# Kernel tuning notes

Measured on AMD Instinct MI355X. Metric: run time of the kernel, lower is better.

Reference implementation:

```python
import jax, jax.numpy as jnp
import numpy as np
import math

EMBED = 1024
HEADS = 16
HEAD_DIM = EMBED // HEADS


def setup_inputs() -> dict:
    key = jax.random.key(0)
    k1, k2, k3 = jax.random.split(key, 3)
    B, C, N = 2, EMBED, 2048
    x = jax.random.normal(k1, (B, C, N), dtype=jnp.float32)
    # Conv1d(kernel_size=1, bias=False) weights, stored as [out_ch, in_ch]
    fan = 1.0 / math.sqrt(EMBED)
    w_qkv = jax.random.uniform(k2, (3 * EMBED, EMBED), dtype=jnp.float32, minval=-fan, maxval=fan)
    w_out = jax.random.uniform(k3, (EMBED, EMBED), dtype=jnp.float32, minval=-fan, maxval=fan)
    return {"x": x, "w_qkv": w_qkv, "w_out": w_out}


def reference(x, w_qkv, w_out):
    B, C, N = x.shape
    H, HD = HEADS, HEAD_DIM
    # 1x1 conv == channel matmul: [B, 3E, N]
    qkv = jnp.einsum('oc,bcn->bon', w_qkv, x)
    # permute -> [B, N, 3E]; reshape splits 3E as (H, 3*HD) per original code
    qkv = qkv.transpose(0, 2, 1).reshape(B, N, H, 3 * HD)
    qkv = qkv.transpose(0, 2, 1, 3)  # [B, H, N, 3*HD]
    q, k, v = jnp.split(qkv, 3, axis=-1)  # each [B, H, N, HD]
    scale = 1.0 / math.sqrt(HD)
    scores = jnp.einsum('bhnd,bhmd->bhnm', q, k) * scale
    weight = jax.nn.softmax(scores, axis=-1)
    vals = jnp.einsum('bhnm,bhmd->bhnd', weight, v)
    vals = vals.transpose(0, 2, 1, 3).reshape(B, N, C)  # [B, N, C]
    y = jnp.einsum('oc,bnc->bon', w_out, vals)  # [B, C, N]
    return y
```

## Files before the change

### kernel.cpp

```cpp
#include <hip/hip_runtime.h>
#include <stdint.h>

typedef unsigned short u16;
typedef __attribute__((ext_vector_type(8))) short bf16x8;
typedef __attribute__((ext_vector_type(4))) float f32x4;

#define NSEQ  2048
#define EMBED 1024
#define NHEAD 16
#define HDIM  64
#define QSCALE 0.1803368801111204f

__device__ __forceinline__ u16 f2bf(float f) {
  uint32_t u = __builtin_bit_cast(uint32_t, f);
  u += 0x7fffu + ((u >> 16) & 1u);
  return (u16)(u >> 16);
}

__device__ __forceinline__ uint32_t pk2(float a, float b) {
  return (uint32_t)f2bf(a) | ((uint32_t)f2bf(b) << 16);
}

__device__ __forceinline__ void gl_lds16(const void* g, void* l) {
  __builtin_amdgcn_global_load_lds(
      (const __attribute__((address_space(1))) void*)g,
      (__attribute__((address_space(3))) void*)l, 16, 0, 0);
}

struct alignas(8) us4 { u16 a, b, c, d; };

__global__ __launch_bounds__(256)
void convertw(const float* __restrict__ wq, const float* __restrict__ wo,
              u16* __restrict__ oq, u16* __restrict__ oo) {
  int idx = blockIdx.x * 256 + threadIdx.x;
  const float* src;
  u16* dst;
  if (idx < 786432) { src = wq; dst = oq; }
  else { idx -= 786432; src = wo; dst = oo; }
  f32x4 v = ((const f32x4*)src)[idx];
  us4 r;
  r.a = f2bf(v[0]); r.b = f2bf(v[1]); r.c = f2bf(v[2]); r.d = f2bf(v[3]);
  ((us4*)dst)[idx] = r;
}

__global__ __launch_bounds__(256)
void transpose_x(const float* __restrict__ x, u16* __restrict__ xT) {
  __shared__ float tile[32][33];
  const int b = blockIdx.z;
  const int n0 = blockIdx.x * 32, c0 = blockIdx.y * 32;
  const int tx = threadIdx.x & 31, ty = threadIdx.x >> 5;
  const float* xb = x + (size_t)b * EMBED * NSEQ;
  #pragma unroll
  for (int k = 0; k < 4; ++k)
    tile[ty + k * 8][tx] = xb[(size_t)(c0 + ty + k * 8) * NSEQ + n0 + tx];
  __syncthreads();
  u16* xTb = xT + (size_t)b * NSEQ * EMBED;
  #pragma unroll
  for (int k = 0; k < 4; ++k)
    xTb[(size_t)(n0 + ty + k * 8) * EMBED + c0 + tx] = f2bf(tile[tx][ty + k * 8]);
}

template<int EPI>
__global__ __launch_bounds__(256, 2)
void gemm_bt(const u16* __restrict__ A, const u16* __restrict__ Bm,
             u16* __restrict__ o_q, u16* __restrict__ o_k, u16* __restrict__ o_vt,
             float* __restrict__ o_f)
{
  __shared__ u16 lA[128 * 64];
  __shared__ u16 lB[128 * 64];
  const int t  = threadIdx.x;
  const int w  = t >> 6;
  const int l  = t & 63;
  const int lr = l & 15, lh = l >> 4;
  const int wm = w >> 1, wn = w & 1;
  const int bz = blockIdx.z;
  const int m0 = blockIdx.x * 128;
  const int n0 = blockIdx.y * 128;

  const u16* Ab = A  + (EPI == 0 ? (size_t)bz * NSEQ * EMBED : (size_t)0);
  const u16* Bb = Bm + (EPI == 0 ? (size_t)0 : (size_t)bz * NSEQ * EMBED);

  f32x4 acc[4][4];
  #pragma unroll
  for (int i = 0; i < 4; ++i)
    #pragma unroll
    for (int j = 0; j < 4; ++j)
      acc[i][j] = (f32x4){0.f, 0.f, 0.f, 0.f};

  const int srow = t >> 3;
  const int slot = t & 7;
  char* ldsA = (char*)lA + (w << 10);
  char* ldsB = (char*)lB + (w << 10);

  for (int k0 = 0; k0 < EMBED; k0 += 64) {
    __syncthreads();
    #pragma unroll
    for (int i = 0; i < 4; ++i) {
      const int row = i * 32 + srow;
      const int sc  = ((slot * 16) ^ ((row & 7) << 4)) >> 1;
      gl_lds16(Ab + (size_t)(m0 + row) * EMBED + k0 + sc, ldsA + i * 4096);
      gl_lds16(Bb + (size_t)(n0 + row) * EMBED + k0 + sc, ldsB + i * 4096);
    }
    __syncthreads();
    #pragma unroll
    for (int kk = 0; kk < 2; ++kk) {
      bf16x8 af[4], bfr[4];
      #pragma unroll
      for (int mr = 0; mr < 4; ++mr) {
        const int row = wm * 64 + mr * 16 + lr;
        const int c2  = (kk * 64 + lh * 16) ^ ((row & 7) << 4);
        af[mr] = *(const bf16x8*)((const char*)lA + row * 128 + c2);
      }
      #pragma unroll
      for (int nc = 0; nc < 4; ++nc) {
        const int row = wn * 64 + nc * 16 + lr;
        const int c2  = (kk * 64 + lh * 16) ^ ((row & 7) << 4);
        bfr[nc] = *(const bf16x8*)((const char*)lB + row * 128 + c2);
      }
      #pragma unroll
      for (int mr = 0; mr < 4; ++mr)
        #pragma unroll
        for (int nc = 0; nc < 4; ++nc)
          acc[mr][nc] = __builtin_amdgcn_mfma_f32_16x16x32_bf16(
              af[mr], bfr[nc], acc[mr][nc], 0, 0, 0);
    }
  }

  if constexpr (EPI == 0) {
    #pragma unroll
    for (int mr = 0; mr < 4; ++mr) {
      #pragma unroll
      for (int nc = 0; nc < 4; ++nc) {
        const int o  = n0 + wn * 64 + nc * 16 + lr;
        const int h  = o / 192;
        const int rr = o - h * 192;
        const size_t bh = (size_t)bz * NHEAD + h;
        #pragma unroll
        for (int r = 0; r < 4; ++r) {
          const int n = m0 + wm * 64 + mr * 16 + lh * 4 + r;
          if (rr < 64)       o_q [(bh * NSEQ + n) * HDIM + rr]         = f2bf(acc[mr][nc][r] * QSCALE);
          else if (rr < 128) o_k [(bh * NSEQ + n) * HDIM + (rr - 64)]  = f2bf(acc[mr][nc][r]);
          else               o_vt[(bh * HDIM + (rr - 128)) * NSEQ + n] = f2bf(acc[mr][nc][r]);
        }
      }
    }
  } else {
    #pragma unroll
    for (int mr = 0; mr < 4; ++mr)
      #pragma unroll
      for (int nc = 0; nc < 4; ++nc)
        #pragma unroll
        for (int r = 0; r < 4; ++r) {
          const int o = m0 + wm * 64 + mr * 16 + lh * 4 + r;
          const int n = n0 + wn * 64 + nc * 16 + lr;
          o_f[((size_t)bz * EMBED + o) * NSEQ + n] = acc[mr][nc][r];
        }
  }
}

__global__ __launch_bounds__(256, 5)
void attn(const u16* __restrict__ Q, const u16* __restrict__ K,
          const u16* __restrict__ Vt, u16* __restrict__ vals)
{
  __shared__ u16 lK[64 * 64], lV[64 * 64], lQP[64 * 64];
  const int t  = threadIdx.x;
  const int w  = t >> 6, l = t & 63;
  const int lr = l & 15, lh = l >> 4;
  const int q0 = blockIdx.x * 64;
  const int bh = blockIdx.y;
  const int b  = bh >> 4, h = bh & 15;
  const size_t qk0 = (size_t)bh * NSEQ * HDIM;
  const size_t vt0 = (size_t)bh * HDIM * NSEQ;
  const int srow = t >> 3, slot = t & 7;
  const int swzr = (lr & 7) << 4;
  char* const pbase = (char*)lQP + (w << 11) + lr * 128;

  #pragma unroll
  for (int i = 0; i < 2; ++i) {
    const int row = i * 32 + srow;
    const int sc  = ((slot * 16) ^ ((row & 7) << 4)) >> 1;
    gl_lds16(Q + qk0 + (size_t)(q0 + row) * HDIM + sc,
             (char*)lQP + i * 4096 + (w << 10));
  }

  f32x4 accO[4];
  #pragma unroll
  for (int i = 0; i < 4; ++i) accO[i] = (f32x4){0.f, 0.f, 0.f, 0.f};
  float m = -1e30f, lsum = 0.f;
  bf16x8 qf[2];

  for (int j0 = 0; j0 < NSEQ; j0 += 64) {
    __syncthreads();
    #pragma unroll
    for (int i = 0; i < 2; ++i) {
      const int row = i * 32 + srow;
      const int sc  = ((slot * 16) ^ ((row & 7) << 4)) >> 1;
      gl_lds16(K  + qk0 + (size_t)(j0 + row) * HDIM + sc,
               (char*)lK + i * 4096 + (w << 10));
      gl_lds16(Vt + vt0 + (size_t)row * NSEQ + j0 + sc,
               (char*)lV + i * 4096 + (w << 10));
    }
    __syncthreads();
    if (j0 == 0) {
      const int qrow = w * 16 + lr;
      #pragma unroll
      for (int kk = 0; kk < 2; ++kk)
        qf[kk] = *(const bf16x8*)((const char*)lQP + qrow * 128 +
                                  ((kk * 64 + lh * 16) ^ ((qrow & 7) << 4)));
    }

    f32x4 accS[4];
    #pragma unroll
    for (int f = 0; f < 4; ++f) accS[f] = (f32x4){0.f, 0.f, 0.f, 0.f};
    #pragma unroll
    for (int kk = 0; kk < 2; ++kk)
      #pragma unroll
      for (int f = 0; f < 4; ++f) {
        const int row = f * 16 + lr;
        const int c2  = (kk * 64 + lh * 16) ^ ((row & 7) << 4);
        bf16x8 kf = *(const bf16x8*)((const char*)lK + row * 128 + c2);
        accS[f] = __builtin_amdgcn_mfma_f32_16x16x32_bf16(kf, qf[kk], accS[f], 0, 0, 0);
      }

    float fm[4];
    #pragma unroll
    for (int f = 0; f < 4; ++f)
      fm[f] = fmaxf(fmaxf(accS[f][0], accS[f][1]), fmaxf(accS[f][2], accS[f][3]));
    float tm = fmaxf(fmaxf(fm[0], fm[1]), fmaxf(fm[2], fm[3]));
    tm = fmaxf(tm, __shfl_xor(tm, 16, 64));
    tm = fmaxf(tm, __shfl_xor(tm, 32, 64));
    const float nm = fmaxf(m, tm);
    const float al = exp2f(m - nm);
    m = nm;

    float psum = 0.f;
    #pragma unroll
    for (int f = 0; f < 4; ++f) {
      const float e0 = exp2f(accS[f][0] - m);
      const float e1 = exp2f(accS[f][1] - m);
      const float e2 = exp2f(accS[f][2] - m);
      const float e3 = exp2f(accS[f][3] - m);
      psum += (e0 + e1) + (e2 + e3);
      uint2 pw;
      pw.x = pk2(e0, e1);
      pw.y = pk2(e2, e3);
      *(uint2*)(pbase + ((f * 32 + lh * 8) ^ swzr)) = pw;
    }
    psum += __shfl_xor(psum, 16, 64);
    psum += __shfl_xor(psum, 32, 64);
    lsum = lsum * al + psum;
    #pragma unroll
    for (int fd = 0; fd < 4; ++fd)
      #pragma unroll
      for (int r = 0; r < 4; ++r)
        accO[fd][r] *= al;

    #pragma unroll
    for (int kk = 0; kk < 2; ++kk) {
      bf16x8 pf = *(const bf16x8*)(pbase + ((kk * 64 + lh * 16) ^ swzr));
      #pragma unroll
      for (int fd = 0; fd < 4; ++fd) {
        const int row = fd * 16 + lr;
        const int c2  = (kk * 64 + lh * 16) ^ ((row & 7) << 4);
        bf16x8 vf = *(const bf16x8*)((const char*)lV + row * 128 + c2);
        accO[fd] = __builtin_amdgcn_mfma_f32_16x16x32_bf16(vf, pf, accO[fd], 0, 0, 0);
      }
    }
  }

  const float rl = 1.0f / lsum;
  const int n = q0 + w * 16 + lr;
  #pragma unroll
  for (int fd = 0; fd < 4; ++fd) {
    uint2 ow;
    ow.x = pk2(accO[fd][0] * rl, accO[fd][1] * rl);
    ow.y = pk2(accO[fd][2] * rl, accO[fd][3] * rl);
    const int c = h * HDIM + fd * 16 + lh * 4;
    *(uint2*)(vals + ((size_t)b * NSEQ + n) * EMBED + c) = ow;
  }
}

extern "C" void kernel_launch(void* const* d_in, const int* in_sizes, int n_in,
                              void* d_out, int out_size, void* d_ws, size_t ws_size,
                              hipStream_t stream) {
  const float* x    = (const float*)d_in[0];
  const float* wqkv = (const float*)d_in[1];
  const float* wout = (const float*)d_in[2];
  float* y = (float*)d_out;
  char* ws = (char*)d_ws;

  u16* b_wqkv = (u16*)(ws);
  u16* b_wout = (u16*)(ws + 6291456);
  u16* b_xT   = (u16*)(ws + 8388608);
  u16* b_Q    = (u16*)(ws + 16777216);
  u16* b_K    = (u16*)(ws + 25165824);
  u16* b_Vt   = (u16*)(ws + 33554432);
  u16* b_vals = (u16*)(ws + 41943040);

  convertw<<<4096, 256, 0, stream>>>(wqkv, wout, b_wqkv, b_wout);
  transpose_x<<<dim3(64, 32, 2), 256, 0, stream>>>(x, b_xT);
  gemm_bt<0><<<dim3(16, 24, 2), 256, 0, stream>>>(b_xT, b_wqkv, b_Q, b_K, b_Vt, nullptr);
  attn<<<dim3(32, 32), 256, 0, stream>>>(b_Q, b_K, b_Vt, b_vals);
  gemm_bt<1><<<dim3(8, 16, 2), 256, 0, stream>>>(b_wout, b_vals, nullptr, nullptr, nullptr, y);
}
```

Before: 221.1 us.

## Double-buffer K/V tiles in attention with lazy softmax rescale and hardware bf16 pack

Prefetches the next K/V tile into a second LDS buffer while computing on the current one, cutting one barrier per iteration. Softmax rescaling of the accumulator is skipped unless the running max grows by more than a threshold. f32-to-bf16 packing uses the hardware v_cvt_pk_bf16_f32 instruction, and MFMA regions are raised in wave priority. Blocks are remapped so neighbouring blocks share K/V across heads, and the occupancy hint drops from 5 to 4 because LDS use is larger.

```diff
diff --git a/kernel.cpp b/kernel.cpp
--- a/kernel.cpp
+++ b/kernel.cpp
@@ -17,8 +17,10 @@
   return (u16)(u >> 16);
 }
 
-__device__ __forceinline__ uint32_t pk2(float a, float b) {
-  return (uint32_t)f2bf(a) | ((uint32_t)f2bf(b) << 16);
+__device__ __forceinline__ uint32_t cvtpk(float a, float b) {
+  uint32_t r;
+  asm("v_cvt_pk_bf16_f32 %0, %1, %2" : "=v"(r) : "v"(a), "v"(b));
+  return r;
 }
 
 __device__ __forceinline__ void gl_lds16(const void* g, void* l) {
@@ -158,16 +160,18 @@
   }
 }
 
-__global__ __launch_bounds__(256, 5)
+__global__ __launch_bounds__(256, 4)
 void attn(const u16* __restrict__ Q, const u16* __restrict__ K,
           const u16* __restrict__ Vt, u16* __restrict__ vals)
 {
-  __shared__ u16 lK[64 * 64], lV[64 * 64], lQP[64 * 64];
+  __shared__ u16 lK[2][64 * 64], lV[2][64 * 64], lQP[64 * 64];
   const int t  = threadIdx.x;
   const int w  = t >> 6, l = t & 63;
   const int lr = l & 15, lh = l >> 4;
-  const int q0 = blockIdx.x * 64;
-  const int bh = blockIdx.y;
+  const int bid = blockIdx.x;
+  const int s   = bid >> 3;
+  const int bh  = (bid & 7) + 8 * (s >> 5);
+  const int q0  = (s & 31) * 64;
   const int b  = bh >> 4, h = bh & 15;
   const size_t qk0 = (size_t)bh * NSEQ * HDIM;
   const size_t vt0 = (size_t)bh * HDIM * NSEQ;
@@ -181,46 +185,58 @@
     const int sc  = ((slot * 16) ^ ((row & 7) << 4)) >> 1;
     gl_lds16(Q + qk0 + (size_t)(q0 + row) * HDIM + sc,
              (char*)lQP + i * 4096 + (w << 10));
+    gl_lds16(K + qk0 + (size_t)row * HDIM + sc,
+             (char*)lK[0] + i * 4096 + (w << 10));
+    gl_lds16(Vt + vt0 + (size_t)row * NSEQ + sc,
+             (char*)lV[0] + i * 4096 + (w << 10));
+  }
+  __syncthreads();
+
+  bf16x8 qf[2];
+  {
+    const int qrow = w * 16 + lr;
+    #pragma unroll
+    for (int kk = 0; kk < 2; ++kk)
+      qf[kk] = *(const bf16x8*)((const char*)lQP + qrow * 128 +
+                                ((kk * 64 + lh * 16) ^ ((qrow & 7) << 4)));
   }
 
   f32x4 accO[4];
   #pragma unroll
   for (int i = 0; i < 4; ++i) accO[i] = (f32x4){0.f, 0.f, 0.f, 0.f};
   float m = -1e30f, lsum = 0.f;
-  bf16x8 qf[2];
+  int cur = 0;
 
   for (int j0 = 0; j0 < NSEQ; j0 += 64) {
-    __syncthreads();
-    #pragma unroll
-    for (int i = 0; i < 2; ++i) {
-      const int row = i * 32 + srow;
-      const int sc  = ((slot * 16) ^ ((row & 7) << 4)) >> 1;
-      gl_lds16(K  + qk0 + (size_t)(j0 + row) * HDIM + sc,
-               (char*)lK + i * 4096 + (w << 10));
-      gl_lds16(Vt + vt0 + (size_t)row * NSEQ + j0 + sc,
-               (char*)lV + i * 4096 + (w << 10));
-    }
-    __syncthreads();
-    if (j0 == 0) {
-      const int qrow = w * 16 + lr;
-      #pragma unroll
-      for (int kk = 0; kk < 2; ++kk)
-        qf[kk] = *(const bf16x8*)((const char*)lQP + qrow * 128 +
-                                  ((kk * 64 + lh * 16) ^ ((qrow & 7) << 4)));
-    }
+    const int jn = j0 + 64;
+    if (jn < NSEQ) {
+      char* nk = (char*)lK[cur ^ 1];
+      char* nv = (char*)lV[cur ^ 1];
+      #pragma unroll
+      for (int i = 0; i < 2; ++i) {
+        const int row = i * 32 + srow;
+        const int sc  = ((slot * 16) ^ ((row & 7) << 4)) >> 1;
+        gl_lds16(K  + qk0 + (size_t)(jn + row) * HDIM + sc, nk + i * 4096 + (w << 10));
+        gl_lds16(Vt + vt0 + (size_t)row * NSEQ + jn + sc,   nv + i * 4096 + (w << 10));
+      }
+    }
+    const char* kb = (const char*)lK[cur];
+    const char* vb = (const char*)lV[cur];
 
     f32x4 accS[4];
     #pragma unroll
     for (int f = 0; f < 4; ++f) accS[f] = (f32x4){0.f, 0.f, 0.f, 0.f};
+    __builtin_amdgcn_s_setprio(1);
     #pragma unroll
     for (int kk = 0; kk < 2; ++kk)
       #pragma unroll
       for (int f = 0; f < 4; ++f) {
         const int row = f * 16 + lr;
         const int c2  = (kk * 64 + lh * 16) ^ ((row & 7) << 4);
-        bf16x8 kf = *(const bf16x8*)((const char*)lK + row * 128 + c2);
+        bf16x8 kf = *(const bf16x8*)(kb + row * 128 + c2);
         accS[f] = __builtin_amdgcn_mfma_f32_16x16x32_bf16(kf, qf[kk], accS[f], 0, 0, 0);
       }
+    __builtin_amdgcn_s_setprio(0);
 
     float fm[4];
     #pragma unroll
@@ -229,9 +245,17 @@
     float tm = fmaxf(fmaxf(fm[0], fm[1]), fmaxf(fm[2], fm[3]));
     tm = fmaxf(tm, __shfl_xor(tm, 16, 64));
     tm = fmaxf(tm, __shfl_xor(tm, 32, 64));
-    const float nm = fmaxf(m, tm);
-    const float al = exp2f(m - nm);
-    m = nm;
+
+    if (tm > m + 8.f) {
+      const float al = exp2f(m - tm);
+      lsum *= al;
+      #pragma unroll
+      for (int fd = 0; fd < 4; ++fd)
+        #pragma unroll
+        for (int r = 0; r < 4; ++r)
+          accO[fd][r] *= al;
+      m = tm;
+    }
 
     float psum = 0.f;
     #pragma unroll
@@ -242,19 +266,15 @@
       const float e3 = exp2f(accS[f][3] - m);
       psum += (e0 + e1) + (e2 + e3);
       uint2 pw;
-      pw.x = pk2(e0, e1);
-      pw.y = pk2(e2, e3);
+      pw.x = cvtpk(e0, e1);
+      pw.y = cvtpk(e2, e3);
       *(uint2*)(pbase + ((f * 32 + lh * 8) ^ swzr)) = pw;
     }
     psum += __shfl_xor(psum, 16, 64);
     psum += __shfl_xor(psum, 32, 64);
-    lsum = lsum * al + psum;
-    #pragma unroll
-    for (int fd = 0; fd < 4; ++fd)
-      #pragma unroll
-      for (int r = 0; r < 4; ++r)
-        accO[fd][r] *= al;
-
+    lsum += psum;
+
+    __builtin_amdgcn_s_setprio(1);
     #pragma unroll
     for (int kk = 0; kk < 2; ++kk) {
       bf16x8 pf = *(const bf16x8*)(pbase + ((kk * 64 + lh * 16) ^ swzr));
@@ -262,10 +282,14 @@
       for (int fd = 0; fd < 4; ++fd) {
         const int row = fd * 16 + lr;
         const int c2  = (kk * 64 + lh * 16) ^ ((row & 7) << 4);
-        bf16x8 vf = *(const bf16x8*)((const char*)lV + row * 128 + c2);
+        bf16x8 vf = *(const bf16x8*)(vb + row * 128 + c2);
         accO[fd] = __builtin_amdgcn_mfma_f32_16x16x32_bf16(vf, pf, accO[fd], 0, 0, 0);
       }
     }
+    __builtin_amdgcn_s_setprio(0);
+
+    __syncthreads();
+    cur ^= 1;
   }
 
   const float rl = 1.0f / lsum;
@@ -273,8 +297,8 @@
   #pragma unroll
   for (int fd = 0; fd < 4; ++fd) {
     uint2 ow;
-    ow.x = pk2(accO[fd][0] * rl, accO[fd][1] * rl);
-    ow.y = pk2(accO[fd][2] * rl, accO[fd][3] * rl);
+    ow.x = cvtpk(accO[fd][0] * rl, accO[fd][1] * rl);
+    ow.y = cvtpk(accO[fd][2] * rl, accO[fd][3] * rl);
     const int c = h * HDIM + fd * 16 + lh * 4;
     *(uint2*)(vals + ((size_t)b * NSEQ + n) * EMBED + c) = ow;
   }
@@ -300,6 +324,6 @@
   convertw<<<4096, 256, 0, stream>>>(wqkv, wout, b_wqkv, b_wout);
   transpose_x<<<dim3(64, 32, 2), 256, 0, stream>>>(x, b_xT);
   gemm_bt<0><<<dim3(16, 24, 2), 256, 0, stream>>>(b_xT, b_wqkv, b_Q, b_K, b_Vt, nullptr);
-  attn<<<dim3(32, 32), 256, 0, stream>>>(b_Q, b_K, b_Vt, b_vals);
+  attn<<<1024, 256, 0, stream>>>(b_Q, b_K, b_Vt, b_vals);
   gemm_bt<1><<<dim3(8, 16, 2), 256, 0, stream>>>(b_wout, b_vals, nullptr, nullptr, nullptr, y);
 }
```

New measurement: 215.2 us. 1.03x faster.
